# Performance work log

Measured on AMD Instinct MI355X. Metric: run time of the kernel, lower is better.

## Reference

```python
import jax, jax.numpy as jnp
import numpy as np

INFTY_APPROX = 1e30
LAM = 10000.0


def sinusoid_embs(length, width):
    # Transformer-XL sinusoidal embeddings, flipped so row 0 encodes the
    # largest relative distance (length-1), matching the rel_shift convention.
    pos = jnp.arange(length, dtype=jnp.float32)
    inv_lams = 1.0 / (LAM ** (jnp.arange(0, width, 2, dtype=jnp.float32) / width))
    pre = pos[:, None] * inv_lams[None, :]                 # [T, width//2]
    cat = jnp.concatenate([jnp.sin(pre), jnp.cos(pre)], axis=-1)  # [T, width]
    return jnp.flip(cat, axis=0)


def rel_shift(x):
    # x: [B, T, T] -> out[b,i,j] = x[b, i, j - i + T - 1] (XL pad/reshape trick)
    b, t, _ = x.shape
    x = jnp.pad(x, ((0, 0), (0, 0), (1, 0)))               # [B, T, T+1]
    x = x.reshape(b, t + 1, t)[:, 1:, :]                   # [B, T, T]
    return x


def setup_inputs() -> dict:
    B, T, D, K, V = 2, 4096, 1024, 128, 2048
    key = jax.random.key(0)
    ks = jax.random.split(key, 10)
    s_d = 1.0 / np.sqrt(D)
    s_v = 1.0 / np.sqrt(V)
    return {
        'x':    jax.random.normal(ks[0], (B, T, D), dtype=jnp.float32),
        'g_ln': jnp.ones((D,), dtype=jnp.float32),
        'W_q':  s_d * jax.random.normal(ks[1], (D, K), dtype=jnp.float32),
        'W_k':  s_d * jax.random.normal(ks[2], (D, K), dtype=jnp.float32),
        'W_v':  s_d * jax.random.normal(ks[3], (D, V), dtype=jnp.float32),
        'W_g':  s_d * jax.random.normal(ks[4], (D, V), dtype=jnp.float32),
        'W_r':  s_d * jax.random.normal(ks[5], (D, K), dtype=jnp.float32),
        'xl_u': 0.02 * jax.random.normal(ks[6], (K,), dtype=jnp.float32),
        'xl_v': 0.02 * jax.random.normal(ks[7], (K,), dtype=jnp.float32),
        'W_o':  s_v * jax.random.normal(ks[8], (V, D), dtype=jnp.float32),
    }


def reference(x, g_ln, W_q, W_k, W_v, W_g, W_r, xl_u, xl_v, W_o):
    B, T, D = x.shape
    K = W_q.shape[-1]
    tau = jnp.asarray(K, x.dtype) ** 0.5

    # RMSNorm input layernorm
    x_tilde = x * jax.lax.rsqrt(jnp.mean(jnp.square(x), axis=-1, keepdims=True) + 1e-6)
    x_tilde = x_tilde * g_ln

    # QKVG projections; queries pre-scaled by 1/tau (producer-side scaling)
    q = (x_tilde @ W_q) / tau                              # [B, T, K]
    k = x_tilde @ W_k                                      # [B, T, K]
    v = x_tilde @ W_v                                      # [B, T, V]

    # XL relative-position bias inputs
    xl_r = sinusoid_embs(T, D) @ W_r                       # [T, K]

    # AC term (content) and BD term (position) with XL u/v biases
    scores_ac = jnp.einsum('bik,bjk->bij', q + xl_u, k)    # [B, T, T]
    scores_bd = jnp.einsum('bik,jk->bij', q + xl_v, xl_r)  # [B, T, T]
    scores_bd = rel_shift(scores_bd)

    scores = scores_ac + scores_bd
    keep = jnp.tril(jnp.ones((T, T), dtype=bool))          # causal keep mask
    scores = scores - jnp.asarray(INFTY_APPROX, x.dtype) * jnp.logical_not(keep)

    w = jax.nn.softmax(scores, axis=-1)                    # [B, T, T]
    wv = jnp.einsum('bij,bjv->biv', w, v)                  # [B, T, V]

    # SHGA gating (GAU-style silu gate)
    wv = wv * jax.nn.silu(x_tilde @ W_g)

    res = wv @ W_o                                         # [B, T, D]
    return res
```

## Files before the change

kernel.cpp:

```cpp
#include <hip/hip_runtime.h>
#include <hip/hip_bf16.h>
#include <stdint.h>

typedef __attribute__((ext_vector_type(4))) float f32x4;
typedef __attribute__((ext_vector_type(8))) short s16x8;
typedef __attribute__((ext_vector_type(8))) unsigned short u16x8;
typedef __attribute__((ext_vector_type(4))) unsigned short u16x4;

static __device__ __forceinline__ float b2f(unsigned short u) {
  union { unsigned int i; float f; } v; v.i = ((unsigned int)u) << 16; return v.f;
}
static __device__ __forceinline__ unsigned short f2b(float f) {
  unsigned int x = __float_as_uint(f);
  return (unsigned short)((x + 0x7fffu + ((x >> 16) & 1u)) >> 16);
}

typedef __attribute__((address_space(1))) const void gconst_t;
typedef __attribute__((address_space(3))) void lds_t;
static __device__ __forceinline__ void gload_lds16(const void* g, void* l) {
  __builtin_amdgcn_global_load_lds((gconst_t*)g, (lds_t*)l, 16, 0, 0);
}

template<int N>
static __device__ __forceinline__ void vmwait() {
  asm volatile("s_waitcnt vmcnt(%0)" :: "n"(N) : "memory");
}
static __device__ __forceinline__ void barmid() {
  __builtin_amdgcn_sched_barrier(0);
  __builtin_amdgcn_s_barrier();
  asm volatile("s_waitcnt lgkmcnt(0)" ::: "memory");
  __builtin_amdgcn_sched_barrier(0);
}
static __device__ __forceinline__ void barend() {
  __builtin_amdgcn_sched_barrier(0);
  __builtin_amdgcn_s_barrier();
}

struct GemmP {
  const unsigned short* A; const unsigned short* B; void* C;
  long sA, sB, sC;
  int M, N, K, lda, ldb, ldc;
  int causal, kend_mode, swapxy;
  int gxs, gys, qchunk;
  const float* uvec; const float* vvec;
  unsigned short* qv_out; unsigned short* kk_out; float invtau;
  const float* rinv; const unsigned short* gate;
  const unsigned short* bds; float* stats;
};

template<int PAIR, int EPI>
__launch_bounds__(512, 2)
__global__ void gemm8p128_k(GemmP p) {
  __shared__ unsigned short L[3][3][8192];
  const int lin = (int)blockIdx.x + (int)gridDim.x * ((int)blockIdx.y + (int)gridDim.y * (int)blockIdx.z);
  const int wg = (lin & 7) * p.qchunk + (lin >> 3);
  const int xx = wg & ((1 << p.gxs) - 1);
  const int yy = (wg >> p.gxs) & ((1 << p.gys) - 1);
  const int b  = wg >> (p.gxs + p.gys);
  const int jj = PAIR ? yy : (p.swapxy ? xx : yy);
  const int j0 = jj * 128;
  const unsigned short* Bg0 = p.B + (long)b * p.sB + (long)j0 * p.ldb;
  const int lda = p.lda, ldb = p.ldb;

  const int tid = threadIdx.x;
  const int w = tid >> 6, l = tid & 63;
  const int wr = w >> 1, wc = w & 1;
  const int fr = l & 15, fq = l >> 4;

  const int sx = (fr & 7) << 4;
  const int abase = ((((wr & 1) << 13) + (fr << 7) + (fq << 4))) ^ sx;
  const int bbase = (((wc << 13) + (fr << 7) + (fq << 4))) ^ sx;

  const int passes = PAIR ? 2 : 1;
  for (int ps = 0; ps < passes; ++ps) {
    const int ii = PAIR ? (ps ? xx : (15 - xx)) : (p.swapxy ? yy : xx);
    const int i0 = ii * 256;
    const unsigned short* Ag = p.A + (long)b * p.sA + (long)i0 * lda;
    const int kend = p.kend_mode ? min(p.K, i0 + 256) : p.K;
    const int NT = kend >> 6;

    auto stA = [&](int slot, int h, int t) {
#pragma unroll
      for (int u = 0; u < 2; ++u) {
        const int sl = u * 512 + tid, r = sl >> 3, g = sl & 7;
        const int gs = g ^ (r & 7);
        gload_lds16(Ag + (long)(h * 128 + r) * lda + t * 64 + gs * 8, &L[slot][h][sl * 8]);
      }
    };
    auto stB = [&](int slot, int bh, int t) {
      const int r = tid >> 3, g = tid & 7;
      const int rloc = bh * 64 + r;
      const int gs = g ^ (rloc & 7);
      gload_lds16(Bg0 + (long)rloc * ldb + t * 64 + gs * 8, &L[slot][2][bh * 4096 + tid * 8]);
    };

    f32x4 acc[4][4];
#pragma unroll
    for (int m = 0; m < 4; ++m)
#pragma unroll
      for (int n = 0; n < 4; ++n) acc[m][n] = (f32x4){0.f, 0.f, 0.f, 0.f};
    s16x8 a[4][2], bA[2][2], bB[2][2];

    auto rdA = [&](int slot) {
      const int reg = wr >> 1;
#pragma unroll
      for (int m = 0; m < 4; ++m)
#pragma unroll
        for (int ks = 0; ks < 2; ++ks)
          a[m][ks] = *(const s16x8*)((const char*)&L[slot][reg][0] +
                                     ((abase ^ (ks << 6)) | (m << 11)));
    };
    auto rdB = [&](int slot, int nq, s16x8 (&bb)[2][2]) {
#pragma unroll
      for (int n = 0; n < 2; ++n)
#pragma unroll
        for (int ks = 0; ks < 2; ++ks)
          bb[n][ks] = *(const s16x8*)((const char*)&L[slot][2][0] +
                                      ((bbase ^ (ks << 6)) | ((nq * 2 + n) << 11)));
    };
    auto mm = [&](int nq, s16x8 (&bb)[2][2]) {
#pragma unroll
      for (int m = 0; m < 4; ++m)
#pragma unroll
        for (int n = 0; n < 2; ++n)
#pragma unroll
          for (int ks = 0; ks < 2; ++ks)
            acc[m][nq * 2 + n] =
                __builtin_amdgcn_mfma_f32_16x16x32_bf16(a[m][ks], bb[n][ks],
                                                        acc[m][nq * 2 + n], 0, 0, 0);
    };

    stA(0, 0, 0); stB(0, 0, 0); stA(0, 1, 0); stB(0, 1, 0);
    stA(1, 0, 1); stB(1, 0, 1); stA(1, 1, 1); stB(1, 1, 1);
    vmwait<6>();
    barend();

    int s = 0;
    for (int t = 0; t < NT; ++t) {
      int s2 = s + 2; if (s2 >= 3) s2 -= 3;
      const bool pf = (t + 2 < NT);
      rdA(s); rdB(s, 0, bA); rdB(s, 1, bB);
      if (pf) { stA(s2, 0, t + 2); stB(s2, 0, t + 2); stA(s2, 1, t + 2); stB(s2, 1, t + 2); }
      barmid();
      __builtin_amdgcn_s_setprio(1);
      mm(0, bA); mm(1, bB);
      __builtin_amdgcn_s_setprio(0);
      if (t == NT - 2) vmwait<0>(); else if (t < NT - 2) vmwait<6>();
      barend();
      s = (s + 1 == 3) ? 0 : s + 1;
    }

    const int rb = i0 + wr * 64 + fq * 4;
    const int cb = j0 + wc * 64 + fr;
    const long tb = (long)b * p.sC;
#pragma unroll
    for (int m = 0; m < 4; ++m)
#pragma unroll
      for (int n = 0; n < 4; ++n) {
        const int col = cb + n * 16;
#pragma unroll
        for (int e = 0; e < 4; ++e) {
          const int row = rb + m * 16 + e;
          const float val = acc[m][n][e];
          if constexpr (EPI == 0) {
            ((unsigned short*)p.C)[tb + (long)row * p.ldc + col] = f2b(val);
          } else if constexpr (EPI == 1) {
            ((float*)p.C)[tb + (long)row * p.ldc + col] = val;
          } else if constexpr (EPI == 2) {
            ((unsigned short*)p.C)[tb + (long)row * p.ldc + col] =
                f2b(val / (1.f + __expf(-val)));
          } else {
            const long coff = tb + (long)row * p.ldc + col;
            const float g = b2f(p.gate[coff]);
            const float r = p.rinv[b * p.M + row];
            ((unsigned short*)p.C)[coff] = f2b(val * r * g);
          }
        }
      }
  }
}

template<int NREP, int EPI>
__launch_bounds__(512, 4)
__global__ void gemm2p_k(GemmP p) {
  constexpr int BN = NREP * 64;
  constexpr int CB = NREP / 2;
  constexpr int LPT = 1 + CB;
  const int lin = (int)blockIdx.x + (((int)blockIdx.y + (int)blockIdx.z * (int)gridDim.y) << p.gxs);
  const int wg = (lin & 7) * p.qchunk + (lin >> 3);
  const int ii = wg & ((1 << p.gxs) - 1);
  const int jj = (wg >> p.gxs) & ((1 << p.gys) - 1);
  const int b  = wg >> (p.gxs + p.gys);
  const int i0 = ii * 128, j0 = jj * BN;
  if (p.causal && j0 > i0 + 127) return;
  const unsigned short* Ag = p.A + (long)b * p.sA + (long)i0 * p.lda;
  const unsigned short* Bg = p.B + (long)b * p.sB + (long)j0 * p.ldb;
  const int NT = p.K >> 5;

  __shared__ unsigned short As[3][128 * 32];
  __shared__ unsigned short Bs[3][BN * 32];

  const int tid = threadIdx.x;
  const int w = tid >> 6, l = tid & 63;
  const int wr = w >> 2, wc = w & 3;
  const int lrow = l >> 2;
  const int swz = ((l & 3) ^ ((l >> 3) & 3)) * 8;

  auto stage = [&](int t, int bi) {
    gload_lds16(Ag + (long)(w * 16 + lrow) * p.lda + t * 32 + swz, &As[bi][w * 512]);
#pragma unroll
    for (int i = 0; i < CB; ++i) {
      const int c = w * CB + i;
      gload_lds16(Bg + (long)(c * 16 + lrow) * p.ldb + t * 32 + swz, &Bs[bi][c * 512]);
    }
  };

  f32x4 acc[4][NREP];
#pragma unroll
  for (int m = 0; m < 4; ++m)
#pragma unroll
    for (int n = 0; n < NREP; ++n) acc[m][n] = (f32x4){0.f, 0.f, 0.f, 0.f};

  const int fr = l & 15, fq = l >> 4;
  const int rg = (fq ^ ((fr >> 1) & 3)) * 8;
  const int aoff = (wr * 64 + fr) * 32 + rg;
  const int boff = (wc * (NREP * 16) + fr) * 32 + rg;

  stage(0, 0);
  if (NT > 1) stage(1, 1);

  int bi = 0;
  for (int t = 0; t < NT; ++t) {
    if (t == NT - 1) vmwait<0>(); else vmwait<LPT>();
    __builtin_amdgcn_s_barrier();
    __builtin_amdgcn_sched_barrier(0);
    const unsigned short* as = &As[bi][0];
    const unsigned short* bs = &Bs[bi][0];
    s16x8 af[4], bf[NREP];
#pragma unroll
    for (int m = 0; m < 4; ++m) af[m] = *(const s16x8*)(as + aoff + m * 512);
#pragma unroll
    for (int n = 0; n < NREP; ++n) bf[n] = *(const s16x8*)(bs + boff + n * 512);
    if (t + 2 < NT) {
      int bi2 = bi + 2; if (bi2 >= 3) bi2 -= 3;
      stage(t + 2, bi2);
    }
    __builtin_amdgcn_s_setprio(1);
#pragma unroll
    for (int m = 0; m < 4; ++m)
#pragma unroll
      for (int n = 0; n < NREP; ++n)
        acc[m][n] = __builtin_amdgcn_mfma_f32_16x16x32_bf16(af[m], bf[n], acc[m][n], 0, 0, 0);
    __builtin_amdgcn_s_setprio(0);
    bi = (bi + 1 == 3) ? 0 : bi + 1;
  }

  const int rbase = i0 + wr * 64 + fq * 4;
  const int cbase = j0 + wc * (NREP * 16) + fr;
  const long tb = (long)b * p.sC;

  if constexpr (EPI == 6) {
    float psum[16];
#pragma unroll
    for (int t = 0; t < 16; ++t) psum[t] = 0.f;
#pragma unroll
    for (int m = 0; m < 4; ++m)
#pragma unroll
      for (int n = 0; n < NREP; ++n) {
        const int col = cbase + n * 16;
#pragma unroll
        for (int e = 0; e < 4; ++e) {
          const int row = rbase + m * 16 + e;
          const long o = tb + (long)row * p.ldc + col;
          float ev = 0.f;
          if (col <= row) {
            const float s = acc[m][n][e] + b2f(p.bds[o]);
            ev = __expf(fminf(s, 60.f));
          }
          ((unsigned short*)p.C)[o] = f2b(ev);
          psum[m * 4 + e] += ev;
        }
      }
#pragma unroll
    for (int t = 0; t < 16; ++t) {
      float v = psum[t];
      v += __shfl_xor(v, 1); v += __shfl_xor(v, 2);
      v += __shfl_xor(v, 4); v += __shfl_xor(v, 8);
      psum[t] = v;
    }
    if (fr == 0) {
#pragma unroll
      for (int t = 0; t < 16; ++t) {
        const int row = rbase + (t >> 2) * 16 + (t & 3);
        p.stats[((long)(b * p.M + row) * 16 + jj) * 4 + wc] = psum[t];
      }
    }
    return;
  }

#pragma unroll
  for (int m = 0; m < 4; ++m)
#pragma unroll
    for (int n = 0; n < NREP; ++n) {
      const int col = cbase + n * 16;
#pragma unroll
      for (int e = 0; e < 4; ++e) {
        const int row = rbase + m * 16 + e;
        if constexpr (EPI == 5) {
          if (col <= row)
            ((unsigned short*)p.C)[tb + (long)row * p.ldc + (row - col)] = f2b(acc[m][n][e]);
        }
      }
    }
}

template<int EPI>
__launch_bounds__(256)
__global__ void gemm_bt_k(GemmP p) {
  const int i0 = blockIdx.x * 128;
  const int j0 = blockIdx.y * 128;
  const unsigned short* A = p.A + (long)i0 * p.lda;
  const unsigned short* B = p.B + (long)j0 * p.ldb;

  __shared__ unsigned short As[128 * 32];
  __shared__ unsigned short Bs[128 * 32];

  const int tid = threadIdx.x;
  const int w = tid >> 6, l = tid & 63;
  const int wr = w >> 1, wc = w & 1;

  f32x4 acc[4][4];
#pragma unroll
  for (int m = 0; m < 4; ++m)
#pragma unroll
    for (int n = 0; n < 4; ++n) acc[m][n] = (f32x4){0.f, 0.f, 0.f, 0.f};

  const int srow = (l >> 2);
  const int scol = ((l & 3) ^ ((l >> 3) & 3)) * 8;
  const unsigned short* ga0 = A + (long)(w * 16 + srow) * p.lda + scol;
  const unsigned short* ga1 = A + (long)((w + 4) * 16 + srow) * p.lda + scol;
  const unsigned short* gb0 = B + (long)(w * 16 + srow) * p.ldb + scol;
  const unsigned short* gb1 = B + (long)((w + 4) * 16 + srow) * p.ldb + scol;
  unsigned short* la0 = As + w * 512;
  unsigned short* la1 = As + (w + 4) * 512;
  unsigned short* lb0 = Bs + w * 512;
  unsigned short* lb1 = Bs + (w + 4) * 512;

  const int rg = ((l >> 4) ^ (((l & 15) >> 1) & 3)) * 8;
  const unsigned short* ap = As + ((wr * 64) + (l & 15)) * 32 + rg;
  const unsigned short* bp = Bs + ((wc * 64) + (l & 15)) * 32 + rg;

  for (int k0 = 0; k0 < p.K; k0 += 32) {
    gload_lds16(ga0 + k0, la0);
    gload_lds16(ga1 + k0, la1);
    gload_lds16(gb0 + k0, lb0);
    gload_lds16(gb1 + k0, lb1);
    __syncthreads();
    s16x8 af[4], bfr[4];
#pragma unroll
    for (int m = 0; m < 4; ++m) af[m] = *(const s16x8*)(ap + m * 16 * 32);
#pragma unroll
    for (int n = 0; n < 4; ++n) bfr[n] = *(const s16x8*)(bp + n * 16 * 32);
#pragma unroll
    for (int m = 0; m < 4; ++m)
#pragma unroll
      for (int n = 0; n < 4; ++n)
        acc[m][n] = __builtin_amdgcn_mfma_f32_16x16x32_bf16(af[m], bfr[n], acc[m][n], 0, 0, 0);
    __syncthreads();
  }

  const int rbase = i0 + wr * 64 + (l >> 4) * 4;
  const int cbase = j0 + wc * 64 + (l & 15);
#pragma unroll
  for (int m = 0; m < 4; ++m)
#pragma unroll
    for (int n = 0; n < 4; ++n) {
      const int col = cbase + n * 16;
#pragma unroll
      for (int e = 0; e < 4; ++e) {
        const int row = rbase + m * 16 + e;
        const float val = acc[m][n][e];
        if constexpr (EPI == 0) {
          ((unsigned short*)p.C)[(long)row * p.ldc + col] = f2b(val);
        } else if constexpr (EPI == 3) {
          if (j0 == 0) {
            const float q = val * p.invtau;
            const long o = (long)row * 128 + col;
            ((unsigned short*)p.C)[o] = f2b(q + p.uvec[col]);
            p.qv_out[o] = f2b(q + p.vvec[col]);
          } else {
            p.kk_out[(long)row * 128 + (col - 128)] = f2b(val);
          }
        }
      }
    }
}

__launch_bounds__(256)
__global__ void rmsnorm_k(const float* __restrict__ x, const float* __restrict__ g,
                          unsigned short* __restrict__ xt) {
  const long row = blockIdx.x;
  const float* xr = x + row * 1024;
  const int t = threadIdx.x;
  const float4 v = ((const float4*)xr)[t];
  float ss = v.x * v.x + v.y * v.y + v.z * v.z + v.w * v.w;
#pragma unroll
  for (int o = 1; o < 64; o <<= 1) ss += __shfl_xor(ss, o);
  __shared__ float wsum[4];
  if ((t & 63) == 0) wsum[t >> 6] = ss;
  __syncthreads();
  const float tot = wsum[0] + wsum[1] + wsum[2] + wsum[3];
  const float r = 1.0f / sqrtf(tot * (1.0f / 1024.0f) + 1e-6f);
  const float4 gv = ((const float4*)g)[t];
  u16x4 o;
  o.x = f2b(v.x * r * gv.x); o.y = f2b(v.y * r * gv.y);
  o.z = f2b(v.z * r * gv.z); o.w = f2b(v.w * r * gv.w);
  ((u16x4*)(xt + row * 1024))[t] = o;
}

__launch_bounds__(256)
__global__ void sinemb_k(unsigned short* __restrict__ emb) {
  const int idx = blockIdx.x * 256 + threadIdx.x;
  const int t = idx >> 10, w = idx & 1023;
  const int h = w & 511;
  const float inv = __expf(-(float)h * (9.2103403719761836f / 512.0f));
  const float pre = (float)t * inv;
  const float val = (w < 512) ? sinf(pre) : cosf(pre);
  emb[idx] = f2b(val);
}

struct TcP {
  const float* in[6];
  unsigned short* out[6];
  int R[6], C[6];
  int start[7];
};
__launch_bounds__(256)
__global__ void transcast6_k(TcP tc) {
  __shared__ float tile[32][33];
  const int bid = blockIdx.x;
  int m = 0;
#pragma unroll
  for (int i = 0; i < 6; ++i) if (bid >= tc.start[i + 1]) m = i + 1;
  const int local = bid - tc.start[m];
  const int R = tc.R[m], C = tc.C[m];
  const int tc_c = C >> 5;
  const int cx = local % tc_c, ry = local / tc_c;
  const int c0 = cx * 32, r0 = ry * 32;
  const float* in = tc.in[m];
  unsigned short* out = tc.out[m];
  const int tx = threadIdx.x & 31, ty = threadIdx.x >> 5;
#pragma unroll
  for (int k = 0; k < 4; ++k)
    tile[ty + k * 8][tx] = in[(long)(r0 + ty + k * 8) * C + c0 + tx];
  __syncthreads();
#pragma unroll
  for (int k = 0; k < 4; ++k)
    out[(long)(c0 + ty + k * 8) * R + r0 + tx] = f2b(tile[tx][ty + k * 8]);
}

__global__ void rowinv_k(const float* __restrict__ stats, float* __restrict__ rinv,
                         int T, int BT) {
  const int idx = blockIdx.x * 256 + threadIdx.x;
  if (idx >= BT) return;
  const int i = idx & (T - 1);
  const int nt = (i >> 8) + 1;
  const float* st = stats + (long)idx * 64;
  float s = 0.f;
  for (int jt = 0; jt < nt; ++jt)
    s += st[jt * 4] + st[jt * 4 + 1] + st[jt * 4 + 2] + st[jt * 4 + 3];
  rinv[idx] = 1.0f / s;
}

extern "C" void kernel_launch(void* const* d_in, const int* in_sizes, int n_in,
                              void* d_out, int out_size, void* d_ws, size_t ws_size,
                              hipStream_t stream) {
  const float* x    = (const float*)d_in[0];
  const float* g_ln = (const float*)d_in[1];
  const float* W_q  = (const float*)d_in[2];
  const float* W_k  = (const float*)d_in[3];
  const float* W_v  = (const float*)d_in[4];
  const float* W_g  = (const float*)d_in[5];
  const float* W_r  = (const float*)d_in[6];
  const float* xl_u = (const float*)d_in[7];
  const float* xl_v = (const float*)d_in[8];
  const float* W_o  = (const float*)d_in[9];
  float* out = (float*)d_out;

  const int B = 2, T = 4096, D = 1024, K = 128, V = 2048;
  const int BT = B * T;

  char* ws = (char*)d_ws;
  size_t off = 0;
  auto alloc = [&](size_t bytes) -> void* {
    void* p = ws + off; off += (bytes + 255) & ~(size_t)255; return p;
  };
  unsigned short* XT   = (unsigned short*)alloc((size_t)BT * D * 2);
  unsigned short* WQKT = (unsigned short*)alloc((size_t)256 * D * 2);
  unsigned short* WVT  = (unsigned short*)alloc((size_t)V * D * 2);
  unsigned short* WGT  = (unsigned short*)alloc((size_t)V * D * 2);
  unsigned short* WRT  = (unsigned short*)alloc((size_t)K * D * 2);
  unsigned short* WOT  = (unsigned short*)alloc((size_t)D * V * 2);
  unsigned short* QU   = (unsigned short*)alloc((size_t)BT * K * 2);
  unsigned short* QV   = (unsigned short*)alloc((size_t)BT * K * 2);
  unsigned short* KKb  = (unsigned short*)alloc((size_t)BT * K * 2);
  unsigned short* RR   = (unsigned short*)alloc((size_t)T * K * 2);
  unsigned short* VVT  = (unsigned short*)alloc((size_t)V * BT * 2);
  unsigned short* GATE = (unsigned short*)alloc((size_t)BT * V * 2);
  float* STATS         = (float*)alloc((size_t)BT * 64 * 4);
  float* RINV          = (float*)alloc((size_t)BT * 4);
  unsigned short* EBUF = (unsigned short*)alloc((size_t)B * T * T * 2);
  unsigned short* BD2  = (unsigned short*)alloc((size_t)B * T * T * 2);
  unsigned short* EMB  = BD2;
  unsigned short* WVG  = BD2;
  if (off > ws_size) return;
  (void)in_sizes; (void)n_in; (void)out_size;

  const float invtau = 0.08838834764831845f;

  {
    TcP tc{};
    const float* ins[6]  = {W_q, W_k, W_v, W_g, W_r, W_o};
    unsigned short* os[6] = {WQKT, WQKT + (size_t)K * D, WVT, WGT, WRT, WOT};
    const int Rs[6] = {D, D, D, D, D, V};
    const int Cs[6] = {K, K, V, V, K, D};
    int acc = 0;
    for (int i = 0; i < 6; ++i) {
      tc.in[i] = ins[i]; tc.out[i] = os[i]; tc.R[i] = Rs[i]; tc.C[i] = Cs[i];
      tc.start[i] = acc; acc += (Rs[i] / 32) * (Cs[i] / 32);
    }
    tc.start[6] = acc;
    transcast6_k<<<acc, 256, 0, stream>>>(tc);
  }
  rmsnorm_k<<<BT, 256, 0, stream>>>(x, g_ln, XT);
  sinemb_k<<<(T * D) / 256, 256, 0, stream>>>(EMB);

  {
    GemmP p{}; p.A = XT; p.B = WQKT; p.C = QU;
    p.M = BT; p.N = 256; p.K = D; p.lda = D; p.ldb = D; p.ldc = K;
    p.uvec = xl_u; p.vvec = xl_v; p.qv_out = QV; p.kk_out = KKb; p.invtau = invtau;
    gemm_bt_k<3><<<dim3(BT / 128, 2, 1), 256, 0, stream>>>(p);
  }
  {
    GemmP p{}; p.A = EMB; p.B = WRT; p.C = RR;
    p.M = T; p.N = K; p.K = D; p.lda = D; p.ldb = D; p.ldc = K;
    gemm_bt_k<0><<<dim3(T / 128, 1, 1), 256, 0, stream>>>(p);
  }
  {
    GemmP p{}; p.A = WVT; p.B = XT; p.C = VVT;
    p.M = V; p.N = BT; p.K = D; p.lda = D; p.ldb = D; p.ldc = BT;
    p.gxs = 3; p.gys = 6; p.qchunk = 64; p.swapxy = 0;
    gemm8p128_k<0, 0><<<dim3(8, 64, 1), 512, 0, stream>>>(p);
  }
  {
    GemmP p{}; p.A = XT; p.B = WGT; p.C = GATE;
    p.M = BT; p.N = V; p.K = D; p.lda = D; p.ldb = D; p.ldc = V;
    p.gxs = 5; p.gys = 4; p.qchunk = 64; p.swapxy = 0;
    gemm8p128_k<0, 2><<<dim3(32, 16, 1), 512, 0, stream>>>(p);
  }
  {
    GemmP p{}; p.A = QV; p.B = RR; p.C = BD2;
    p.sA = (long)T * K; p.sB = 0; p.sC = (long)T * T;
    p.M = T; p.N = T; p.K = K; p.lda = K; p.ldb = K; p.ldc = T; p.causal = 1;
    p.gxs = 5; p.gys = 4; p.qchunk = 128;
    gemm2p_k<4, 5><<<dim3(32, 16, B), 512, 0, stream>>>(p);
  }
  {
    GemmP p{}; p.A = QU; p.B = KKb; p.C = EBUF;
    p.sA = (long)T * K; p.sB = (long)T * K; p.sC = (long)T * T;
    p.M = T; p.N = T; p.K = K; p.lda = K; p.ldb = K; p.ldc = T; p.causal = 1;
    p.bds = BD2; p.stats = STATS;
    p.gxs = 5; p.gys = 4; p.qchunk = 128;
    gemm2p_k<4, 6><<<dim3(32, 16, B), 512, 0, stream>>>(p);
  }
  rowinv_k<<<BT / 256, 256, 0, stream>>>(STATS, RINV, T, BT);
  {
    GemmP p{}; p.A = EBUF; p.B = VVT; p.C = WVG;
    p.sA = (long)T * T; p.sB = T; p.sC = (long)T * V;
    p.M = T; p.N = V; p.K = T; p.lda = T; p.ldb = BT; p.ldc = V;
    p.kend_mode = 1; p.rinv = RINV; p.gate = GATE;
    p.gxs = 3; p.gys = 4; p.qchunk = 32;
    gemm8p128_k<1, 4><<<dim3(8, 16, 2), 512, 0, stream>>>(p);
  }
  {
    GemmP p{}; p.A = WVG; p.B = WOT; p.C = out;
    p.M = BT; p.N = D; p.K = V; p.lda = V; p.ldb = V; p.ldc = D;
    p.gxs = 3; p.gys = 5; p.qchunk = 32; p.swapxy = 1;
    gemm8p128_k<0, 1><<<dim3(8, 32, 1), 512, 0, stream>>>(p);
  }
}
```

Baseline: 389.5 us.

## Add 4-stage pipelined 256x128 GEMM kernel for causal PV product

Adds a new GEMM kernel for the attention-weights × V product. It uses 256 threads, 256x128 tiles with K=32 steps and a 4-deep LDS ring filled via global_load_lds. A fragments are double-buffered in registers so LDS reads overlap the MFMAs, with lgkmcnt waits and setprio around the MFMA block. Tiles are walked in reverse row order so the heavier causal tiles are scheduled first. It replaces the previous paired 8-wave kernel for this stage. In exchange it uses more registers per thread and runs at one workgroup per CU.

```diff
diff --git a/kernel.cpp b/kernel.cpp
--- a/kernel.cpp
+++ b/kernel.cpp
@@ -24,6 +24,11 @@
 template<int N>
 static __device__ __forceinline__ void vmwait() {
   asm volatile("s_waitcnt vmcnt(%0)" :: "n"(N) : "memory");
+}
+template<int N>
+static __device__ __forceinline__ void lgkm() {
+  asm volatile("s_waitcnt lgkmcnt(%0)" :: "n"(N) : "memory");
+  __builtin_amdgcn_sched_barrier(0);
 }
 static __device__ __forceinline__ void barmid() {
   __builtin_amdgcn_sched_barrier(0);
@@ -47,6 +52,129 @@
   const float* rinv; const unsigned short* gate;
   const unsigned short* bds; float* stats;
 };
+
+template<int EPI>
+__launch_bounds__(256, 1)
+__global__ void gemmpl_k(GemmP p) {
+  __shared__ unsigned short LA[4][256 * 32];
+  __shared__ unsigned short LB[4][128 * 32];
+  const int lin = (int)blockIdx.x + (int)gridDim.x * ((int)blockIdx.y + (int)gridDim.y * (int)blockIdx.z);
+  const int wg = (lin & 7) * p.qchunk + (lin >> 3);
+  int ii = wg & ((1 << p.gxs) - 1);
+  const int jj = (wg >> p.gxs) & ((1 << p.gys) - 1);
+  const int b  = wg >> (p.gxs + p.gys);
+  if (p.kend_mode) ii = (1 << p.gxs) - 1 - ii;
+  const int i0 = ii * 256, j0 = jj * 128;
+  const unsigned short* Ag = p.A + (long)b * p.sA + (long)i0 * p.lda;
+  const unsigned short* Bg = p.B + (long)b * p.sB + (long)j0 * p.ldb;
+  const int lda = p.lda, ldb = p.ldb;
+  const int kend = p.kend_mode ? min(p.K, i0 + 256) : p.K;
+  const int NT = kend >> 5;
+
+  const int tid = threadIdx.x;
+  const int w = tid >> 6, l = tid & 63;
+  const int wr = w >> 1, wc = w & 1;
+  const int fr = l & 15, fq = l >> 4;
+
+  auto stage = [&](int t, int s) {
+#pragma unroll
+    for (int u = 0; u < 4; ++u) {
+      const int sl = u * 256 + tid, r = sl >> 2, g = sl & 3;
+      const int gs = g ^ ((r >> 1) & 3);
+      gload_lds16(Ag + (long)r * lda + t * 32 + gs * 8, &LA[s][sl * 8]);
+    }
+#pragma unroll
+    for (int u = 0; u < 2; ++u) {
+      const int sl = u * 256 + tid, r = sl >> 2, g = sl & 3;
+      const int gs = g ^ ((r >> 1) & 3);
+      gload_lds16(Bg + (long)r * ldb + t * 32 + gs * 8, &LB[s][sl * 8]);
+    }
+  };
+
+  f32x4 acc[8][4];
+#pragma unroll
+  for (int m = 0; m < 8; ++m)
+#pragma unroll
+    for (int n = 0; n < 4; ++n) acc[m][n] = (f32x4){0.f, 0.f, 0.f, 0.f};
+
+  const int rg = (fq ^ ((fr >> 1) & 3)) * 8;
+  const int aoff = (wr * 128 + fr) * 32 + rg;
+  const int boff = (wc * 64 + fr) * 32 + rg;
+
+  s16x8 aE[8], aO[8], bf[4];
+
+  auto rdA = [&](int s, s16x8 (&a)[8]) {
+#pragma unroll
+    for (int m = 0; m < 8; ++m)
+      a[m] = *(const s16x8*)(&LA[s][0] + aoff + m * 512);
+  };
+  auto rdB = [&](int s) {
+#pragma unroll
+    for (int n = 0; n < 4; ++n)
+      bf[n] = *(const s16x8*)(&LB[s][0] + boff + n * 512);
+  };
+  auto mm = [&](s16x8 (&a)[8]) {
+    __builtin_amdgcn_s_setprio(1);
+#pragma unroll
+    for (int m = 0; m < 8; ++m)
+#pragma unroll
+      for (int n = 0; n < 4; ++n)
+        acc[m][n] = __builtin_amdgcn_mfma_f32_16x16x32_bf16(a[m], bf[n], acc[m][n], 0, 0, 0);
+    __builtin_amdgcn_s_setprio(0);
+  };
+
+  stage(0, 0);
+  if (NT > 1) stage(1, 1);
+  if (NT > 2) stage(2, 2);
+  if (NT > 2) vmwait<6>(); else vmwait<0>();
+  barend();
+  rdA(0, aE);
+
+  for (int t = 0; t < NT; ++t) {
+    const int scur = t & 3, snxt = (t + 1) & 3;
+    const bool hasN = (t + 1 < NT);
+    if (!(t & 1)) {
+      rdB(scur);
+      if (hasN) rdA(snxt, aO);
+      if (t + 3 < NT) stage(t + 3, (t + 3) & 3);
+      if (hasN) lgkm<8>(); else lgkm<0>();
+      mm(aE);
+    } else {
+      rdB(scur);
+      if (hasN) rdA(snxt, aE);
+      if (t + 3 < NT) stage(t + 3, (t + 3) & 3);
+      if (hasN) lgkm<8>(); else lgkm<0>();
+      mm(aO);
+    }
+    if (hasN) {
+      if (t + 3 < NT) vmwait<6>(); else vmwait<0>();
+      barend();
+    }
+  }
+
+  const int rb = i0 + wr * 128 + fq * 4;
+  const int cb = j0 + wc * 64 + fr;
+  const long tb = (long)b * p.sC;
+#pragma unroll
+  for (int m = 0; m < 8; ++m)
+#pragma unroll
+    for (int n = 0; n < 4; ++n) {
+      const int col = cb + n * 16;
+#pragma unroll
+      for (int e = 0; e < 4; ++e) {
+        const int row = rb + m * 16 + e;
+        const float val = acc[m][n][e];
+        if constexpr (EPI == 1) {
+          ((float*)p.C)[tb + (long)row * p.ldc + col] = val;
+        } else {
+          const long coff = tb + (long)row * p.ldc + col;
+          const float g = b2f(p.gate[coff]);
+          const float r = p.rinv[b * p.M + row];
+          ((unsigned short*)p.C)[coff] = f2b(val * r * g);
+        }
+      }
+    }
+}
 
 template<int PAIR, int EPI>
 __launch_bounds__(512, 2)
@@ -579,8 +707,8 @@
     p.sA = (long)T * T; p.sB = T; p.sC = (long)T * V;
     p.M = T; p.N = V; p.K = T; p.lda = T; p.ldb = BT; p.ldc = V;
     p.kend_mode = 1; p.rinv = RINV; p.gate = GATE;
-    p.gxs = 3; p.gys = 4; p.qchunk = 32;
-    gemm8p128_k<1, 4><<<dim3(8, 16, 2), 512, 0, stream>>>(p);
+    p.gxs = 4; p.gys = 4; p.qchunk = 64;
+    gemmpl_k<4><<<dim3(16, 16, 2), 256, 0, stream>>>(p);
   }
   {
     GemmP p{}; p.A = WVG; p.B = WOT; p.C = out;
```

New measurement: 622.5 us. 1.6x slower.
